# Performance work log

Hardware: AMD Instinct MI355X
Metric: run time of the kernel (lower is better)

Reference implementation:

```python
import jax, jax.numpy as jnp
import numpy as np

B, T, D, H, V = 4096, 30, 512, 1024, 128  # words, MAX_WORD_LEN, input_dim, hidden, num_of_chars

def setup_inputs() -> dict:
    key = jax.random.key(0)
    ks = jax.random.split(key, 8)
    x = jax.random.randint(ks[0], (B, T), 0, V)
    emb = jax.random.normal(ks[1], (V, D), jnp.float32)
    s = 1.0 / np.sqrt(H)  # torch LSTMCell default init range
    W_ih = jax.random.uniform(ks[2], (4 * H, D), jnp.float32, -s, s)
    W_hh = jax.random.uniform(ks[3], (4 * H, H), jnp.float32, -s, s)
    b_ih = jax.random.uniform(ks[4], (4 * H,), jnp.float32, -s, s)
    b_hh = jax.random.uniform(ks[5], (4 * H,), jnp.float32, -s, s)
    xav = np.sqrt(2.0 / (B + H))  # xavier_normal_ std for [B,H] state tensors
    h0 = jax.random.normal(ks[6], (B, H), jnp.float32) * xav
    c0 = jax.random.normal(ks[7], (B, H), jnp.float32) * xav
    return {"x": x, "emb": emb, "W_ih": W_ih, "W_hh": W_hh,
            "b_ih": b_ih, "b_hh": b_hh, "h0": h0, "c0": c0}

def reference(x, emb, W_ih, W_hh, b_ih, b_hh, h0, c0):
    xe = emb[x]                       # [B, T, D] char embeddings
    xs = jnp.swapaxes(xe, 0, 1)       # [T, B, D] for scan over time

    def step(carry, xt):
        h, c = carry
        # torch LSTMCell gate order: i, f, g, o
        gates = xt @ W_ih.T + b_ih + h @ W_hh.T + b_hh  # [B, 4H]
        i, f, g, o = jnp.split(gates, 4, axis=-1)
        c = jax.nn.sigmoid(f) * c + jax.nn.sigmoid(i) * jnp.tanh(g)
        h = jax.nn.sigmoid(o) * jnp.tanh(c)
        return (h, c), None

    (h, c), _ = jax.lax.scan(step, (h0, c0), xs)
    return h
```

## Files before the change

kernel.cpp:

```cpp
#include <hip/hip_runtime.h>
#include <hip/hip_bf16.h>

#define BW    4096
#define TT    30
#define DIN   512
#define HD    1024
#define VCH   128
#define G4    4096

typedef __attribute__((ext_vector_type(8))) __bf16 bf16x8;
typedef __attribute__((ext_vector_type(4))) float  f32x4;

__device__ __forceinline__ ushort f2bf(float f) {
    unsigned u = __float_as_uint(f);
    unsigned r = (u + 0x7fffu + ((u >> 16) & 1u)) >> 16;
    return (ushort)r;
}
__device__ __forceinline__ float sigf(float x) { return 1.f / (1.f + __expf(-x)); }
__device__ __forceinline__ float tanhfast(float x) { return 2.f / (1.f + __expf(-2.f * x)) - 1.f; }


__global__ __launch_bounds__(256) void cvt_bf16_kernel(const float* __restrict__ in,
                                                       ushort* __restrict__ out, int n4) {
    int i = blockIdx.x * 256 + threadIdx.x;
    if (i >= n4) return;
    float4 v = ((const float4*)in)[i];
    ushort4 o;
    o.x = f2bf(v.x); o.y = f2bf(v.y); o.z = f2bf(v.z); o.w = f2bf(v.w);
    ((ushort4*)out)[i] = o;
}

__global__ __launch_bounds__(256) void init_hc_kernel(const float* __restrict__ h0,
                                                      const float* __restrict__ c0,
                                                      ushort* __restrict__ hb,
                                                      float* __restrict__ c, int n4) {
    int i = blockIdx.x * 256 + threadIdx.x;
    if (i >= n4) return;
    float4 v = ((const float4*)h0)[i];
    ushort4 o;
    o.x = f2bf(v.x); o.y = f2bf(v.y); o.z = f2bf(v.z); o.w = f2bf(v.w);
    ((ushort4*)hb)[i] = o;
    ((float4*)c)[i] = ((const float4*)c0)[i];
}

__global__ __launch_bounds__(256) void proj_emb_kernel(const float* __restrict__ emb,
                                                       const float* __restrict__ W_ih,
                                                       const float* __restrict__ b_ih,
                                                       const float* __restrict__ b_hh,
                                                       float* __restrict__ pe) {
    __shared__ float se[8][DIN];
    const int j  = blockIdx.x * 256 + threadIdx.x;
    const int c0 = blockIdx.y * 8;
    for (int i = threadIdx.x; i < 8 * DIN; i += 256)
        se[i >> 9][i & (DIN - 1)] = emb[(size_t)c0 * DIN + i];
    __syncthreads();
    const float* wv = W_ih + (size_t)j * DIN;
    float s[8];
#pragma unroll
    for (int cc = 0; cc < 8; ++cc) s[cc] = 0.f;
    for (int k = 0; k < DIN; k += 4) {
        float4 w4 = *(const float4*)&wv[k];
#pragma unroll
        for (int cc = 0; cc < 8; ++cc)
            s[cc] += se[cc][k] * w4.x + se[cc][k+1] * w4.y + se[cc][k+2] * w4.z + se[cc][k+3] * w4.w;
    }
    const float bias = b_ih[j] + b_hh[j];
    const int g = j >> 10, h = j & 1023;
#pragma unroll
    for (int cc = 0; cc < 8; ++cc)
        pe[(((size_t)(c0 + cc) * HD + h) << 2) + g] = s[cc] + bias;
}


#define GLDS(SRC, DST)                                                                  \
    __builtin_amdgcn_global_load_lds((const __attribute__((address_space(1))) void*)(SRC), \
        (__attribute__((address_space(3))) void*)(DST), 16, 0, 0)

#define STAGE2(AB, SB, SH, SKT)                                                        \
  {                                                                                    \
    ushort* dst0 = &tiles[((((SB)*2 + (AB))*2 + (SH)) * 8192) + w * 1024];             \
    const ushort *s0, *s1;                                                             \
    if ((AB) == 0) {                                                                   \
      s0 = A + aOff0 + (size_t)(SH)*131072 + (size_t)(SKT)*64;                         \
      s1 = A + aOff1 + (size_t)(SH)*131072 + (size_t)(SKT)*64;                         \
    } else {                                                                           \
      s0 = Bt + bOff[SH][0] + (size_t)(SKT)*64;                                        \
      s1 = Bt + bOff[SH][1] + (size_t)(SKT)*64;                                        \
    }                                                                                  \
    GLDS(s0, dst0);                                                                    \
    GLDS(s1, dst0 + 512);                                                              \
  }

#define PHASE(BUF, Q, AB, SB, SH, SKT, VM)                                             \
  {                                                                                    \
    const ushort* aT = &tiles[(((BUF)*2 + 0)*2 + haA) * 8192];                         \
    const ushort* bT = &tiles[(((BUF)*2 + 1)*2 + haB) * 8192];                         \
    if ((Q) == 0) {                                                                    \
      _Pragma("unroll")                                                                \
      for (int n = 0; n < 4; ++n) {                                                    \
        bfr[n][0] = *(const bf16x8*)(bT + hbOff + n*1024 + aoff0);                     \
        bfr[n][1] = *(const bf16x8*)(bT + hbOff + n*1024 + aoff1);                     \
      }                                                                                \
    }                                                                                  \
    bf16x8 a00 = *(const bf16x8*)(aT + (2*(Q)+0)*1024 + aoff0);                        \
    bf16x8 a01 = *(const bf16x8*)(aT + (2*(Q)+0)*1024 + aoff1);                        \
    bf16x8 a10 = *(const bf16x8*)(aT + (2*(Q)+1)*1024 + aoff0);                        \
    bf16x8 a11 = *(const bf16x8*)(aT + (2*(Q)+1)*1024 + aoff1);                        \
    STAGE2(AB, SB, SH, SKT);                                                           \
    __builtin_amdgcn_s_barrier();                                                      \
    asm volatile("s_waitcnt lgkmcnt(0)" ::: "memory");                                 \
    __builtin_amdgcn_s_setprio(1);                                                     \
    _Pragma("unroll")                                                                  \
    for (int n = 0; n < 4; ++n) {                                                      \
      acc[2*(Q)+0][n] = __builtin_amdgcn_mfma_f32_16x16x32_bf16(a00, bfr[n][0], acc[2*(Q)+0][n], 0, 0, 0); \
      acc[2*(Q)+0][n] = __builtin_amdgcn_mfma_f32_16x16x32_bf16(a01, bfr[n][1], acc[2*(Q)+0][n], 0, 0, 0); \
      acc[2*(Q)+1][n] = __builtin_amdgcn_mfma_f32_16x16x32_bf16(a10, bfr[n][0], acc[2*(Q)+1][n], 0, 0, 0); \
      acc[2*(Q)+1][n] = __builtin_amdgcn_mfma_f32_16x16x32_bf16(a11, bfr[n][1], acc[2*(Q)+1][n], 0, 0, 0); \
    }                                                                                  \
    __builtin_amdgcn_s_setprio(0);                                                     \
    if (VM) asm volatile("s_waitcnt vmcnt(4)" ::: "memory");                           \
    __builtin_amdgcn_s_barrier();                                                      \
    asm volatile("" ::: "memory");                                                     \
  }

__global__ __launch_bounds__(512, 2) void gemm_cell_kernel(const ushort* __restrict__ A,
                                                           const ushort* __restrict__ Bt,
                                                           const float* __restrict__ peAll,
                                                           const int* __restrict__ x,
                                                           int t, int last,
                                                           float* __restrict__ c,
                                                           ushort* __restrict__ hbN,
                                                           float* __restrict__ hout) {
    __shared__ ushort tiles[65536];
    __shared__ int xs[256];

    const int orig = blockIdx.x;
    const int xcd = orig & 7, j = orig >> 3;
    const int bm = j >> 1;
    const int bn = (xcd << 1) | (j & 1);

    const int tid = threadIdx.x;
    const int w = tid >> 6, l = tid & 63;
    const int fr = l & 15, hi = l >> 4;
    const int haA = w >> 2;
    const int haB = (w >> 1) & 1;
    const int hbOff = (w & 1) * 4096;

    if (tid < 256) xs[tid] = x[(bm * 256 + tid) * TT + t];
    __syncthreads();

    const int r0 = w * 16 + (l >> 3), r1 = r0 + 8;
    const int csrc = (l & 7) ^ (l >> 3);
    const size_t aOff0 = (size_t)(bm * 256 + r0) * 1024 + csrc * 8;
    const size_t aOff1 = (size_t)(bm * 256 + r1) * 1024 + csrc * 8;
    size_t bOff[2][2];
#pragma unroll
    for (int half = 0; half < 2; ++half) {
        const int ra = half * 128 + r0, rb = half * 128 + r1;
        const int na = ((ra >> 4) & 3) * 1024 + bn * 64 + ((ra >> 6) << 4) + (ra & 15);
        const int nb = ((rb >> 4) & 3) * 1024 + bn * 64 + ((rb >> 6) << 4) + (rb & 15);
        bOff[half][0] = (size_t)na * 1024 + csrc * 8;
        bOff[half][1] = (size_t)nb * 1024 + csrc * 8;
    }

    const int aoff0 = fr * 64 + ((hi) ^ (fr & 7)) * 8;
    const int aoff1 = fr * 64 + ((4 + hi) ^ (fr & 7)) * 8;

    f32x4 acc[8][4];
#pragma unroll
    for (int m = 0; m < 8; ++m)
#pragma unroll
        for (int n = 0; n < 4; ++n) acc[m][n] = 0.f;
    bf16x8 bfr[4][2];

    STAGE2(0, 0, 0, 0);
    STAGE2(0, 0, 1, 0);
    STAGE2(1, 0, 0, 0);
    STAGE2(1, 0, 1, 0);
    STAGE2(1, 1, 0, 1);
    STAGE2(1, 1, 1, 1);
    asm volatile("s_waitcnt vmcnt(4)" ::: "memory");
    __builtin_amdgcn_s_barrier();
    asm volatile("" ::: "memory");

    for (int i = 0; i < 8; ++i) {
        const int k0 = 2 * i;
        PHASE(0, 0, 0, 1, 0, k0 + 1, 0);
        PHASE(0, 1, 0, 1, 1, k0 + 1, 0);
        PHASE(0, 2, 1, 0, 0, (k0 + 2) & 15, 0);
        PHASE(0, 3, 1, 0, 1, (k0 + 2) & 15, 1);
        PHASE(1, 0, 0, 0, 0, (k0 + 2) & 15, 0);
        PHASE(1, 1, 0, 0, 1, (k0 + 2) & 15, 0);
        PHASE(1, 2, 1, 1, 0, (k0 + 3) & 15, 0);
        PHASE(1, 3, 1, 1, 1, (k0 + 3) & 15, 1);
    }
    asm volatile("s_waitcnt vmcnt(0)" ::: "memory");

    const int h_idx = bn * 64 + (w & 3) * 16 + fr;
    const int bloc0 = (w >> 2) * 128 + (hi << 2);
    const int bbase = bm * 256 + bloc0;
    const float4* pe4 = (const float4*)peAll;
#pragma unroll
    for (int m = 0; m < 8; ++m) {
#pragma unroll
        for (int r = 0; r < 4; ++r) {
            const int b = bbase + m * 16 + r;
            const int ch = xs[bloc0 + m * 16 + r];
            const float4 pv = pe4[(size_t)ch * HD + h_idx];
            float I = sigf(acc[m][0][r] + pv.x);
            float F = sigf(acc[m][1][r] + pv.y);
            float G = tanhfast(acc[m][2][r] + pv.z);
            float O = sigf(acc[m][3][r] + pv.w);
            const size_t off = (size_t)b * HD + h_idx;
            const float cn = F * c[off] + I * G;
            const float hn = O * tanhfast(cn);
            c[off] = cn;
            hbN[off] = f2bf(hn);
            if (last) hout[off] = hn;
        }
    }
}

extern "C" void kernel_launch(void* const* d_in, const int* in_sizes, int n_in,
                              void* d_out, int out_size, void* d_ws, size_t ws_size,
                              hipStream_t stream) {
    const int*   x    = (const int*)d_in[0];
    const float* emb  = (const float*)d_in[1];
    const float* W_ih = (const float*)d_in[2];
    const float* W_hh = (const float*)d_in[3];
    const float* b_ih = (const float*)d_in[4];
    const float* b_hh = (const float*)d_in[5];
    const float* h0   = (const float*)d_in[6];
    const float* c0   = (const float*)d_in[7];
    float* out = (float*)d_out;

    char* ws = (char*)d_ws;
    ushort* whh = (ushort*)ws;
    float*  pe  = (float*)(ws + (size_t)8388608);
    ushort* hb0 = (ushort*)(ws + (size_t)(8388608 + 2097152));
    ushort* hb1 = (ushort*)(ws + (size_t)(8388608 + 2097152 + 8388608));
    float*  cbuf = (float*)(ws + (size_t)(8388608 + 2097152 + 8388608 + 8388608));

    cvt_bf16_kernel<<<4096, 256, 0, stream>>>(W_hh, whh, (G4 * HD) / 4);
    proj_emb_kernel<<<dim3(16, 16), 256, 0, stream>>>(emb, W_ih, b_ih, b_hh, pe);
    init_hc_kernel<<<4096, 256, 0, stream>>>(h0, c0, hb0, cbuf, (BW * HD) / 4);

    ushort* hbuf[2] = {hb0, hb1};
    for (int t = 0; t < TT; ++t) {
        gemm_cell_kernel<<<256, 512, 0, stream>>>(
            hbuf[t & 1], whh, pe, x, t, (t == TT - 1) ? 1 : 0,
            cbuf, hbuf[(t & 1) ^ 1], out);
    }
}
```

Measured before the change: 1.625 ms.

## Fuse timestep loop into persistent cooperative kernel with register-resident cell state

Replaces 30 per-timestep gemm_cell launches with one cooperative persistent kernel that loops over time and uses grid.sync between steps. The cell state c now stays in registers across steps instead of being read and written in global memory, and all character indices for the block are loaded into shared memory once. This removes launch overhead and c traffic, in exchange for a grid-wide barrier each step. The larger shared-memory footprint (xsAll) and register pressure may affect whether two blocks still fit per CU for co-residency.

```diff
diff --git a/kernel.cpp b/kernel.cpp
--- a/kernel.cpp
+++ b/kernel.cpp
@@ -1,5 +1,8 @@
 #include <hip/hip_runtime.h>
 #include <hip/hip_bf16.h>
+#include <hip/hip_cooperative_groups.h>
+
+namespace cg = cooperative_groups;
 
 #define BW    4096
 #define TT    30
@@ -30,17 +33,14 @@
     ((ushort4*)out)[i] = o;
 }
 
-__global__ __launch_bounds__(256) void init_hc_kernel(const float* __restrict__ h0,
-                                                      const float* __restrict__ c0,
-                                                      ushort* __restrict__ hb,
-                                                      float* __restrict__ c, int n4) {
+__global__ __launch_bounds__(256) void init_h_kernel(const float* __restrict__ h0,
+                                                     ushort* __restrict__ hb, int n4) {
     int i = blockIdx.x * 256 + threadIdx.x;
     if (i >= n4) return;
     float4 v = ((const float4*)h0)[i];
     ushort4 o;
     o.x = f2bf(v.x); o.y = f2bf(v.y); o.z = f2bf(v.z); o.w = f2bf(v.w);
     ((ushort4*)hb)[i] = o;
-    ((float4*)c)[i] = ((const float4*)c0)[i];
 }
 
 __global__ __launch_bounds__(256) void proj_emb_kernel(const float* __restrict__ emb,
@@ -116,28 +116,28 @@
       acc[2*(Q)+0][n] = __builtin_amdgcn_mfma_f32_16x16x32_bf16(a01, bfr[n][1], acc[2*(Q)+0][n], 0, 0, 0); \
       acc[2*(Q)+1][n] = __builtin_amdgcn_mfma_f32_16x16x32_bf16(a10, bfr[n][0], acc[2*(Q)+1][n], 0, 0, 0); \
       acc[2*(Q)+1][n] = __builtin_amdgcn_mfma_f32_16x16x32_bf16(a11, bfr[n][1], acc[2*(Q)+1][n], 0, 0, 0); \
-    }                                                                                  \
-    __builtin_amdgcn_s_setprio(0);                                                     \
-    if (VM) asm volatile("s_waitcnt vmcnt(4)" ::: "memory");                           \
-    __builtin_amdgcn_s_barrier();                                                      \
-    asm volatile("" ::: "memory");                                                     \
+    }                                                                                   \
+    __builtin_amdgcn_s_setprio(0);                                                      \
+    if (VM) asm volatile("s_waitcnt vmcnt(4)" ::: "memory");                            \
+    __builtin_amdgcn_s_barrier();                                                       \
+    asm volatile("" ::: "memory");                                                      \
   }
 
-__global__ __launch_bounds__(512, 2) void gemm_cell_kernel(const ushort* __restrict__ A,
-                                                           const ushort* __restrict__ Bt,
-                                                           const float* __restrict__ peAll,
-                                                           const int* __restrict__ x,
-                                                           int t, int last,
-                                                           float* __restrict__ c,
-                                                           ushort* __restrict__ hbN,
-                                                           float* __restrict__ hout) {
+__global__ __launch_bounds__(512, 2) void lstm_persist_kernel(
+        const int* __restrict__ x, const ushort* __restrict__ Bt,
+        const float* __restrict__ peAll, ushort* __restrict__ hb0,
+        ushort* __restrict__ hb1, const float* __restrict__ c0,
+        float* __restrict__ hout)
+{
     __shared__ ushort tiles[65536];
-    __shared__ int xs[256];
+    __shared__ int xsAll[256 * TT];
+
+    cg::grid_group grid = cg::this_grid();
 
     const int orig = blockIdx.x;
-    const int xcd = orig & 7, j = orig >> 3;
-    const int bm = j >> 1;
-    const int bn = (xcd << 1) | (j & 1);
+    const int xcd = orig & 7, jj = orig >> 3;
+    const int bm = jj >> 1;
+    const int bn = (xcd << 1) | (jj & 1);
 
     const int tid = threadIdx.x;
     const int w = tid >> 6, l = tid & 63;
@@ -146,7 +146,11 @@
     const int haB = (w >> 1) & 1;
     const int hbOff = (w & 1) * 4096;
 
-    if (tid < 256) xs[tid] = x[(bm * 256 + tid) * TT + t];
+    {
+        const int4* xsrc4 = (const int4*)(x + (size_t)bm * 256 * TT);
+        for (int i = tid; i < (256 * TT) / 4; i += 512)
+            ((int4*)xsAll)[i] = xsrc4[i];
+    }
     __syncthreads();
 
     const int r0 = w * 16 + (l >> 3), r1 = r0 + 8;
@@ -166,57 +170,76 @@
     const int aoff0 = fr * 64 + ((hi) ^ (fr & 7)) * 8;
     const int aoff1 = fr * 64 + ((4 + hi) ^ (fr & 7)) * 8;
 
-    f32x4 acc[8][4];
-#pragma unroll
-    for (int m = 0; m < 8; ++m)
-#pragma unroll
-        for (int n = 0; n < 4; ++n) acc[m][n] = 0.f;
-    bf16x8 bfr[4][2];
-
-    STAGE2(0, 0, 0, 0);
-    STAGE2(0, 0, 1, 0);
-    STAGE2(1, 0, 0, 0);
-    STAGE2(1, 0, 1, 0);
-    STAGE2(1, 1, 0, 1);
-    STAGE2(1, 1, 1, 1);
-    asm volatile("s_waitcnt vmcnt(4)" ::: "memory");
-    __builtin_amdgcn_s_barrier();
-    asm volatile("" ::: "memory");
-
-    for (int i = 0; i < 8; ++i) {
-        const int k0 = 2 * i;
-        PHASE(0, 0, 0, 1, 0, k0 + 1, 0);
-        PHASE(0, 1, 0, 1, 1, k0 + 1, 0);
-        PHASE(0, 2, 1, 0, 0, (k0 + 2) & 15, 0);
-        PHASE(0, 3, 1, 0, 1, (k0 + 2) & 15, 1);
-        PHASE(1, 0, 0, 0, 0, (k0 + 2) & 15, 0);
-        PHASE(1, 1, 0, 0, 1, (k0 + 2) & 15, 0);
-        PHASE(1, 2, 1, 1, 0, (k0 + 3) & 15, 0);
-        PHASE(1, 3, 1, 1, 1, (k0 + 3) & 15, 1);
-    }
-    asm volatile("s_waitcnt vmcnt(0)" ::: "memory");
-
     const int h_idx = bn * 64 + (w & 3) * 16 + fr;
     const int bloc0 = (w >> 2) * 128 + (hi << 2);
     const int bbase = bm * 256 + bloc0;
     const float4* pe4 = (const float4*)peAll;
-#pragma unroll
-    for (int m = 0; m < 8; ++m) {
-#pragma unroll
-        for (int r = 0; r < 4; ++r) {
-            const int b = bbase + m * 16 + r;
-            const int ch = xs[bloc0 + m * 16 + r];
-            const float4 pv = pe4[(size_t)ch * HD + h_idx];
-            float I = sigf(acc[m][0][r] + pv.x);
-            float F = sigf(acc[m][1][r] + pv.y);
-            float G = tanhfast(acc[m][2][r] + pv.z);
-            float O = sigf(acc[m][3][r] + pv.w);
-            const size_t off = (size_t)b * HD + h_idx;
-            const float cn = F * c[off] + I * G;
-            const float hn = O * tanhfast(cn);
-            c[off] = cn;
-            hbN[off] = f2bf(hn);
-            if (last) hout[off] = hn;
+
+    f32x4 cReg[8];
+#pragma unroll
+    for (int m = 0; m < 8; ++m)
+#pragma unroll
+        for (int r = 0; r < 4; ++r)
+            cReg[m][r] = c0[(size_t)(bbase + m * 16 + r) * HD + h_idx];
+
+    bf16x8 bfr[4][2];
+
+    for (int t = 0; t < TT; ++t) {
+        const ushort* A = (t & 1) ? hb1 : hb0;
+        ushort* hbW = (t & 1) ? hb0 : hb1;
+
+        f32x4 acc[8][4];
+#pragma unroll
+        for (int m = 0; m < 8; ++m)
+#pragma unroll
+            for (int n = 0; n < 4; ++n) acc[m][n] = 0.f;
+
+        STAGE2(0, 0, 0, 0);
+        STAGE2(0, 0, 1, 0);
+        STAGE2(1, 0, 0, 0);
+        STAGE2(1, 0, 1, 0);
+        STAGE2(1, 1, 0, 1);
+        STAGE2(1, 1, 1, 1);
+        asm volatile("s_waitcnt vmcnt(4)" ::: "memory");
+        __builtin_amdgcn_s_barrier();
+        asm volatile("" ::: "memory");
+
+        for (int i = 0; i < 8; ++i) {
+            const int k0 = 2 * i;
+            PHASE(0, 0, 0, 1, 0, k0 + 1, 0);
+            PHASE(0, 1, 0, 1, 1, k0 + 1, 0);
+            PHASE(0, 2, 1, 0, 0, (k0 + 2) & 15, 0);
+            PHASE(0, 3, 1, 0, 1, (k0 + 2) & 15, 1);
+            PHASE(1, 0, 0, 0, 0, (k0 + 2) & 15, 0);
+            PHASE(1, 1, 0, 0, 1, (k0 + 2) & 15, 0);
+            PHASE(1, 2, 1, 1, 0, (k0 + 3) & 15, 0);
+            PHASE(1, 3, 1, 1, 1, (k0 + 3) & 15, 1);
+        }
+        asm volatile("s_waitcnt vmcnt(0)" ::: "memory");
+
+#pragma unroll
+        for (int m = 0; m < 8; ++m) {
+#pragma unroll
+            for (int r = 0; r < 4; ++r) {
+                const int bloc = bloc0 + m * 16 + r;
+                const int ch = xsAll[bloc * TT + t];
+                const float4 pv = pe4[(size_t)ch * HD + h_idx];
+                float I = sigf(acc[m][0][r] + pv.x);
+                float F = sigf(acc[m][1][r] + pv.y);
+                float G = tanhfast(acc[m][2][r] + pv.z);
+                float O = sigf(acc[m][3][r] + pv.w);
+                const float cn = F * cReg[m][r] + I * G;
+                cReg[m][r] = cn;
+                const float hn = O * tanhfast(cn);
+                const size_t off = (size_t)(bm * 256 + bloc) * HD + h_idx;
+                hbW[off] = f2bf(hn);
+                if (t == TT - 1) hout[off] = hn;
+            }
+        }
+
+        if (t < TT - 1) {
+            __threadfence();
+            grid.sync();
         }
     }
 }
@@ -239,16 +262,15 @@
     float*  pe  = (float*)(ws + (size_t)8388608);
     ushort* hb0 = (ushort*)(ws + (size_t)(8388608 + 2097152));
     ushort* hb1 = (ushort*)(ws + (size_t)(8388608 + 2097152 + 8388608));
-    float*  cbuf = (float*)(ws + (size_t)(8388608 + 2097152 + 8388608 + 8388608));
 
     cvt_bf16_kernel<<<4096, 256, 0, stream>>>(W_hh, whh, (G4 * HD) / 4);
     proj_emb_kernel<<<dim3(16, 16), 256, 0, stream>>>(emb, W_ih, b_ih, b_hh, pe);
-    init_hc_kernel<<<4096, 256, 0, stream>>>(h0, c0, hb0, cbuf, (BW * HD) / 4);
-
-    ushort* hbuf[2] = {hb0, hb1};
-    for (int t = 0; t < TT; ++t) {
-        gemm_cell_kernel<<<256, 512, 0, stream>>>(
-            hbuf[t & 1], whh, pe, x, t, (t == TT - 1) ? 1 : 0,
-            cbuf, hbuf[(t & 1) ^ 1], out);
-    }
-}
+    init_h_kernel<<<4096, 256, 0, stream>>>(h0, hb0, (BW * HD) / 4);
+
+    const int* xA = x; const ushort* whA = whh; const float* peA = pe;
+    ushort* h0A = hb0; ushort* h1A = hb1; const float* c0A = c0; float* outA = out;
+    void* kargs[] = { (void*)&xA, (void*)&whA, (void*)&peA,
+                      (void*)&h0A, (void*)&h1A, (void*)&c0A, (void*)&outA };
+    hipLaunchCooperativeKernel((const void*)lstm_persist_kernel,
+                               dim3(256), dim3(512), kargs, 0, stream);
+}
```

After: 4.175 ms. 2.57x slower.
